# Performance work log

Measured on AMD Instinct MI355X. Metric: run time of the kernel, lower is better.

The kernel has to match this reference:

```python
import jax, jax.numpy as jnp
import numpy as np

D_MODEL = 1024
D_FF = 4096
EPS = 1e-5


def layer_norm(x, gamma, beta):
    mu = jnp.mean(x, axis=-1, keepdims=True)
    var = jnp.var(x, axis=-1, keepdims=True)
    return (x - mu) * jax.lax.rsqrt(var + EPS) * gamma + beta


def attention(x_q, x_kv, WQ, WK, WV, causal):
    Q = x_q @ WQ          # [B,Sq,D]
    K = x_kv @ WK         # [B,Sk,D]
    V = x_kv @ WV
    scale = 1.0 / jnp.sqrt(jnp.asarray(Q.shape[-1], Q.dtype))
    scores = jnp.einsum('bqd,bkd->bqk', Q, K) * scale
    if causal:
        Sq, Sk = scores.shape[-2], scores.shape[-1]
        mask = jnp.triu(jnp.full((Sq, Sk), -jnp.inf, scores.dtype), k=1)
        scores = scores + mask
    attn = jax.nn.softmax(scores, axis=-1)
    return jnp.einsum('bqk,bkd->bqd', attn, V)


def setup_inputs() -> dict:
    key = jax.random.key(0)
    ks = jax.random.split(key, 16)
    B, S = 4, 2048
    s = 0.02
    inp = {
        'y': jax.random.normal(ks[0], (B, S, D_MODEL), jnp.float32),
        'Z': jax.random.normal(ks[1], (B, S, D_MODEL), jnp.float32),
        'WQ1': jax.random.normal(ks[2], (D_MODEL, D_MODEL), jnp.float32) * s,
        'WK1': jax.random.normal(ks[3], (D_MODEL, D_MODEL), jnp.float32) * s,
        'WV1': jax.random.normal(ks[4], (D_MODEL, D_MODEL), jnp.float32) * s,
        'WQ2': jax.random.normal(ks[5], (D_MODEL, D_MODEL), jnp.float32) * s,
        'WK2': jax.random.normal(ks[6], (D_MODEL, D_MODEL), jnp.float32) * s,
        'WV2': jax.random.normal(ks[7], (D_MODEL, D_MODEL), jnp.float32) * s,
        'W_ff1': jax.random.normal(ks[8], (D_MODEL, D_FF), jnp.float32) * s,
        'b_ff1': jnp.zeros((D_FF,), jnp.float32),
        'W_ff2': jax.random.normal(ks[9], (D_FF, D_MODEL), jnp.float32) * s,
        'b_ff2': jnp.zeros((D_MODEL,), jnp.float32),
        'g1': jnp.ones((D_MODEL,), jnp.float32), 'be1': jnp.zeros((D_MODEL,), jnp.float32),
        'g2': jnp.ones((D_MODEL,), jnp.float32), 'be2': jnp.zeros((D_MODEL,), jnp.float32),
        'g3': jnp.ones((D_MODEL,), jnp.float32), 'be3': jnp.zeros((D_MODEL,), jnp.float32),
    }
    return inp


def reference(y, Z, WQ1, WK1, WV1, WQ2, WK2, WV2, W_ff1, b_ff1, W_ff2, b_ff2,
              g1, be1, g2, be2, g3, be3):
    # masked self-attention + add&norm
    y = layer_norm(y + attention(y, y, WQ1, WK1, WV1, causal=True), g1, be1)
    # cross-attention + add&norm
    y = layer_norm(y + attention(y, Z, WQ2, WK2, WV2, causal=False), g2, be2)
    # FFN + add&norm
    h = jax.nn.relu(y @ W_ff1 + b_ff1) @ W_ff2 + b_ff2
    y = layer_norm(y + h, g3, be3)
    return y
```

## Files before the change

### kernel.cpp

```cpp
#include <hip/hip_runtime.h>
#include <cstddef>

typedef unsigned short u16;
typedef __attribute__((ext_vector_type(8))) short bf16x8;
typedef __attribute__((ext_vector_type(4))) float f32x4;

__device__ __forceinline__ u16 f2bf(float f) {
  union { float f; unsigned u; } x; x.f = f;
  unsigned r = x.u + 0x7fffu + ((x.u >> 16) & 1u);
  return (u16)(r >> 16);
}
__device__ __forceinline__ float bf2f(u16 h) {
  union { unsigned u; float f; } x; x.u = ((unsigned)h) << 16;
  return x.f;
}

__device__ __forceinline__ void gll16(const u16* g, u16* ldsbase) {
  __builtin_amdgcn_global_load_lds(
      (const __attribute__((address_space(1))) void*)g,
      (__attribute__((address_space(3))) void*)ldsbase, 16, 0, 0);
}

__global__ __launch_bounds__(256) void f32_to_bf16(const float* __restrict__ in,
                                                   u16* __restrict__ out, size_t n) {
  size_t i = (size_t)blockIdx.x * 256 + threadIdx.x;
  if (i < n) out[i] = f2bf(in[i]);
}

__global__ __launch_bounds__(256) void transpose_f32_bf16(const float* __restrict__ in,
                                                          u16* __restrict__ out,
                                                          int R, int C) {
  __shared__ float tile[32][33];
  int c0 = blockIdx.x * 32, r0 = blockIdx.y * 32;
  int tx = threadIdx.x & 31, ty = threadIdx.x >> 5;
  #pragma unroll
  for (int i = ty; i < 32; i += 8)
    tile[i][tx] = in[(size_t)(r0 + i) * C + c0 + tx];
  __syncthreads();
  #pragma unroll
  for (int i = ty; i < 32; i += 8)
    out[(size_t)(c0 + i) * R + r0 + tx] = f2bf(tile[tx][i]);
}

enum { EPI_F32 = 0, EPI_BF16 = 1, EPI_BF16_SCALE = 2,
       EPI_BIAS_RELU_BF16 = 3, EPI_BIAS_F32 = 4 };
enum { MODE_FULL = 0, MODE_TRI = 1, MODE_CAUSAL_K = 2 };

template <int EPI, int MODE>
__global__ __launch_bounds__(512) void gemm256(
    const u16* __restrict__ A, const u16* __restrict__ Bt,
    void* __restrict__ C0, const float* __restrict__ bias,
    int K, int lda, int ldb, int ldc,
    long long sA, long long sB, long long sC)
{
  __shared__ __align__(16) u16 lA[2][256 * 64];
  __shared__ __align__(16) u16 lB[2][256 * 64];

  const unsigned gx = gridDim.x, gxy = gridDim.x * gridDim.y;
  unsigned id = blockIdx.x + gx * blockIdx.y + gxy * blockIdx.z;
  const unsigned nb = gxy * gridDim.z;
  unsigned p = id;
  if ((nb & 7u) == 0u) p = (id & 7u) * (nb >> 3) + (id >> 3);
  int z, mi, ni;
  if constexpr (MODE == MODE_TRI) {
    z = (int)(p / gxy);
    int r = (int)(p % gxy);
    int m = 0;
    while ((m + 1) * (m + 2) / 2 <= r) m++;
    mi = m; ni = r - m * (m + 1) / 2;
  } else {
    z = (int)(p / gxy);
    const unsigned rem = p % gxy;
    mi = (int)(rem / gx);
    ni = (int)(rem % gx);
  }
  const int m0 = mi * 256, n0 = ni * 256;

  A  += (long long)z * sA;
  Bt += (long long)z * sB;

  int NT = K >> 6;
  if constexpr (MODE == MODE_CAUSAL_K) NT = (m0 + 256) >> 6;

  const int t    = threadIdx.x;
  const int lane = t & 63;
  const int wave = t >> 6;
  const int wr   = wave >> 2;
  const int wc   = wave & 3;
  const int quad = lane >> 4;
  const int lrow = lane & 15;

  const int srow = lane >> 3;
  const int scol = ((lane & 7) ^ srow) * 8;
  const u16* gAp = A  + (size_t)(m0 + wave * 8 + srow) * lda + scol;
  const u16* gBp = Bt + (size_t)(n0 + wave * 8 + srow) * ldb + scol;
  const size_t a64 = (size_t)64 * lda, b64 = (size_t)64 * ldb;
  const int lw = wave * 512;

  const int pg0 = (quad ^ (lrow & 7)) * 8;
  const int pg1 = pg0 ^ 32;
  const int rA = (wr * 128 + lrow) * 64;
  const int rB = (wc * 64 + lrow) * 64;

  f32x4 acc[8][4];
  const f32x4 zero = {0.f, 0.f, 0.f, 0.f};
  #pragma unroll
  for (int i = 0; i < 8; i++)
    #pragma unroll
    for (int j = 0; j < 4; j++) acc[i][j] = zero;

  auto stage = [&](int b, int s, int kt) {
    const int k = kt * 64;
    if (s == 0) {
      gll16(gBp + k,            &lB[b][lw]);
      gll16(gBp + k + b64,      &lB[b][4096 + lw]);
    } else if (s == 1) {
      gll16(gBp + k + 2 * b64,  &lB[b][8192 + lw]);
      gll16(gBp + k + 3 * b64,  &lB[b][12288 + lw]);
    } else if (s == 2) {
      gll16(gAp + k,            &lA[b][lw]);
      gll16(gAp + k + a64,      &lA[b][4096 + lw]);
    } else {
      gll16(gAp + k + 2 * a64,  &lA[b][8192 + lw]);
      gll16(gAp + k + 3 * a64,  &lA[b][12288 + lw]);
    }
  };

  stage(0, 0, 0); stage(0, 1, 0); stage(0, 2, 0); stage(0, 3, 0);
  if (NT > 1) {
    stage(1, 0, 1); stage(1, 1, 1); stage(1, 2, 1);
    asm volatile("s_waitcnt vmcnt(6)" ::: "memory");
  } else {
    asm volatile("s_waitcnt vmcnt(0)" ::: "memory");
  }
  __builtin_amdgcn_s_barrier();

  bf16x8 af[4][2], bfr[4][2];

  for (int kt = 0; kt < NT; ++kt) {
    const int bsel = kt & 1;
    const u16* sa = &lA[bsel][0];
    const u16* sb = &lB[bsel][0];

    #pragma unroll
    for (int mf = 0; mf < 4; ++mf) {
      af[mf][0] = *(const bf16x8*)(sa + rA + mf * 1024 + pg0);
      af[mf][1] = *(const bf16x8*)(sa + rA + mf * 1024 + pg1);
    }
    if (wc < 2) {
      #pragma unroll
      for (int nf = 0; nf < 4; ++nf) {
        bfr[nf][0] = *(const bf16x8*)(sb + rB + nf * 1024 + pg0);
        bfr[nf][1] = *(const bf16x8*)(sb + rB + nf * 1024 + pg1);
      }
    } else {
      #pragma unroll
      for (int nf = 0; nf < 2; ++nf) {
        bfr[nf][0] = *(const bf16x8*)(sb + rB + nf * 1024 + pg0);
        bfr[nf][1] = *(const bf16x8*)(sb + rB + nf * 1024 + pg1);
      }
    }
    if (kt + 1 < NT) stage(bsel ^ 1, 3, kt + 1);
    __builtin_amdgcn_s_barrier();
    asm volatile("s_waitcnt lgkmcnt(0)" ::: "memory");
    __builtin_amdgcn_sched_barrier(0);
    __builtin_amdgcn_s_setprio(1);
    #pragma unroll
    for (int mf = 0; mf < 4; ++mf)
      #pragma unroll
      for (int nf = 0; nf < 2; ++nf) {
        acc[mf][nf] = __builtin_amdgcn_mfma_f32_16x16x32_bf16(bfr[nf][0], af[mf][0], acc[mf][nf], 0, 0, 0);
        acc[mf][nf] = __builtin_amdgcn_mfma_f32_16x16x32_bf16(bfr[nf][1], af[mf][1], acc[mf][nf], 0, 0, 0);
      }
    __builtin_amdgcn_s_setprio(0);
    __builtin_amdgcn_s_barrier();

    if (wc >= 2) {
      #pragma unroll
      for (int nf = 2; nf < 4; ++nf) {
        bfr[nf][0] = *(const bf16x8*)(sb + rB + nf * 1024 + pg0);
        bfr[nf][1] = *(const bf16x8*)(sb + rB + nf * 1024 + pg1);
      }
    }
    if (kt + 2 < NT) stage(bsel, 0, kt + 2);
    __builtin_amdgcn_s_barrier();
    asm volatile("s_waitcnt lgkmcnt(0)" ::: "memory");
    __builtin_amdgcn_sched_barrier(0);
    __builtin_amdgcn_s_setprio(1);
    #pragma unroll
    for (int mf = 0; mf < 4; ++mf)
      #pragma unroll
      for (int nf = 2; nf < 4; ++nf) {
        acc[mf][nf] = __builtin_amdgcn_mfma_f32_16x16x32_bf16(bfr[nf][0], af[mf][0], acc[mf][nf], 0, 0, 0);
        acc[mf][nf] = __builtin_amdgcn_mfma_f32_16x16x32_bf16(bfr[nf][1], af[mf][1], acc[mf][nf], 0, 0, 0);
      }
    __builtin_amdgcn_s_setprio(0);
    __builtin_amdgcn_s_barrier();

    #pragma unroll
    for (int mf = 0; mf < 4; ++mf) {
      af[mf][0] = *(const bf16x8*)(sa + rA + (mf + 4) * 1024 + pg0);
      af[mf][1] = *(const bf16x8*)(sa + rA + (mf + 4) * 1024 + pg1);
    }
    if (kt + 2 < NT) stage(bsel, 1, kt + 2);
    __builtin_amdgcn_s_barrier();
    asm volatile("s_waitcnt lgkmcnt(0)" ::: "memory");
    __builtin_amdgcn_sched_barrier(0);
    __builtin_amdgcn_s_setprio(1);
    #pragma unroll
    for (int mf = 0; mf < 4; ++mf)
      #pragma unroll
      for (int nf = 2; nf < 4; ++nf) {
        acc[mf + 4][nf] = __builtin_amdgcn_mfma_f32_16x16x32_bf16(bfr[nf][0], af[mf][0], acc[mf + 4][nf], 0, 0, 0);
        acc[mf + 4][nf] = __builtin_amdgcn_mfma_f32_16x16x32_bf16(bfr[nf][1], af[mf][1], acc[mf + 4][nf], 0, 0, 0);
      }
    __builtin_amdgcn_s_setprio(0);
    __builtin_amdgcn_s_barrier();

    if (kt + 2 < NT) {
      stage(bsel, 2, kt + 2);
      asm volatile("s_waitcnt vmcnt(6)" ::: "memory");
    } else if (kt + 1 < NT) {
      asm volatile("s_waitcnt vmcnt(0)" ::: "memory");
    }
    __builtin_amdgcn_s_barrier();
    __builtin_amdgcn_s_setprio(1);
    #pragma unroll
    for (int mf = 0; mf < 4; ++mf)
      #pragma unroll
      for (int nf = 0; nf < 2; ++nf) {
        acc[mf + 4][nf] = __builtin_amdgcn_mfma_f32_16x16x32_bf16(bfr[nf][0], af[mf][0], acc[mf + 4][nf], 0, 0, 0);
        acc[mf + 4][nf] = __builtin_amdgcn_mfma_f32_16x16x32_bf16(bfr[nf][1], af[mf][1], acc[mf + 4][nf], 0, 0, 0);
      }
    __builtin_amdgcn_s_setprio(0);
    __builtin_amdgcn_s_barrier();
  }

  const size_t zoff = (size_t)((long long)z * sC);
  #pragma unroll
  for (int mf = 0; mf < 8; ++mf) {
    #pragma unroll
    for (int nf = 0; nf < 4; ++nf) {
      const size_t m  = (size_t)(m0 + wr * 128 + mf * 16 + lrow);
      const size_t nc = (size_t)(n0 + wc * 64 + nf * 16 + quad * 4);
      const size_t idx = zoff + m * (size_t)ldc + nc;
      f32x4 v = acc[mf][nf];
      if constexpr (EPI == EPI_F32) {
        *(float4*)((float*)C0 + idx) = make_float4(v[0], v[1], v[2], v[3]);
      } else if constexpr (EPI == EPI_BF16) {
        ushort4 o; o.x = f2bf(v[0]); o.y = f2bf(v[1]); o.z = f2bf(v[2]); o.w = f2bf(v[3]);
        *(ushort4*)((u16*)C0 + idx) = o;
      } else if constexpr (EPI == EPI_BF16_SCALE) {
        ushort4 o;
        o.x = f2bf(v[0] * 0.03125f); o.y = f2bf(v[1] * 0.03125f);
        o.z = f2bf(v[2] * 0.03125f); o.w = f2bf(v[3] * 0.03125f);
        *(ushort4*)((u16*)C0 + idx) = o;
      } else if constexpr (EPI == EPI_BIAS_RELU_BF16) {
        const float4 bb = *(const float4*)(bias + nc);
        float y0 = v[0] + bb.x, y1 = v[1] + bb.y, y2 = v[2] + bb.z, y3 = v[3] + bb.w;
        ushort4 o;
        o.x = f2bf(y0 > 0.f ? y0 : 0.f); o.y = f2bf(y1 > 0.f ? y1 : 0.f);
        o.z = f2bf(y2 > 0.f ? y2 : 0.f); o.w = f2bf(y3 > 0.f ? y3 : 0.f);
        *(ushort4*)((u16*)C0 + idx) = o;
      } else {
        const float4 bb = *(const float4*)(bias + nc);
        *(float4*)((float*)C0 + idx) =
            make_float4(v[0] + bb.x, v[1] + bb.y, v[2] + bb.z, v[3] + bb.w);
      }
    }
  }
}

__global__ __launch_bounds__(256) void softmax_bf16(u16* __restrict__ SP, int causal) {
  __shared__ float red[8];
  const int row = blockIdx.x;
  const int q = row & 2047;
  u16* p = SP + (size_t)row * 2048;
  const int t = threadIdx.x;
  const int base = t * 8;
  const int limit = causal ? (q + 1) : 2048;

  uint4 raw = *(const uint4*)(p + base);
  unsigned w[4] = {raw.x, raw.y, raw.z, raw.w};
  float v[8];
  #pragma unroll
  for (int j = 0; j < 4; j++) {
    union { unsigned u; float f; } lo, hi;
    lo.u = w[j] << 16; hi.u = w[j] & 0xffff0000u;
    v[2 * j] = lo.f; v[2 * j + 1] = hi.f;
  }
  #pragma unroll
  for (int j = 0; j < 8; j++) if (base + j >= limit) v[j] = -3.4e38f;

  float mx = v[0];
  #pragma unroll
  for (int j = 1; j < 8; j++) mx = fmaxf(mx, v[j]);
  #pragma unroll
  for (int o = 32; o > 0; o >>= 1) mx = fmaxf(mx, __shfl_down(mx, o));
  if ((t & 63) == 0) red[t >> 6] = mx;
  __syncthreads();
  mx = fmaxf(fmaxf(red[0], red[1]), fmaxf(red[2], red[3]));

  float s = 0.f;
  #pragma unroll
  for (int j = 0; j < 8; j++) { float e = __expf(v[j] - mx); v[j] = e; s += e; }
  #pragma unroll
  for (int o = 32; o > 0; o >>= 1) s += __shfl_down(s, o);
  if ((t & 63) == 0) red[4 + (t >> 6)] = s;
  __syncthreads();
  const float inv = 1.f / (red[4] + red[5] + red[6] + red[7]);

  unsigned o4[4];
  #pragma unroll
  for (int j = 0; j < 4; j++)
    o4[j] = (unsigned)f2bf(v[2 * j] * inv) | ((unsigned)f2bf(v[2 * j + 1] * inv) << 16);
  *(uint4*)(p + base) = make_uint4(o4[0], o4[1], o4[2], o4[3]);
}

template <int ABF>
__global__ __launch_bounds__(256) void ln_residual(const void* __restrict__ a_,
                                                   const float* __restrict__ b,
                                                   const float* __restrict__ g,
                                                   const float* __restrict__ be,
                                                   float* __restrict__ outf,
                                                   u16* __restrict__ outb) {
  __shared__ float red[8];
  const size_t base = (size_t)blockIdx.x * 1024;
  const int t = threadIdx.x;
  const int i0 = t * 4;

  float va[4];
  if constexpr (ABF) {
    const ushort4 h = *(const ushort4*)((const u16*)a_ + base + i0);
    va[0] = bf2f(h.x); va[1] = bf2f(h.y); va[2] = bf2f(h.z); va[3] = bf2f(h.w);
  } else {
    const float4 f = *(const float4*)((const float*)a_ + base + i0);
    va[0] = f.x; va[1] = f.y; va[2] = f.z; va[3] = f.w;
  }
  const float4 vb = *(const float4*)(b + base + i0);
  float v[4] = {va[0] + vb.x, va[1] + vb.y, va[2] + vb.z, va[3] + vb.w};

  float s = v[0] + v[1] + v[2] + v[3];
  #pragma unroll
  for (int o = 32; o > 0; o >>= 1) s += __shfl_down(s, o);
  if ((t & 63) == 0) red[t >> 6] = s;
  __syncthreads();
  const float mean = (red[0] + red[1] + red[2] + red[3]) * (1.f / 1024.f);

  float qq = 0.f;
  #pragma unroll
  for (int i = 0; i < 4; i++) { float d = v[i] - mean; qq += d * d; }
  #pragma unroll
  for (int o = 32; o > 0; o >>= 1) qq += __shfl_down(qq, o);
  if ((t & 63) == 0) red[4 + (t >> 6)] = qq;
  __syncthreads();
  const float rstd = rsqrtf((red[4] + red[5] + red[6] + red[7]) * (1.f / 1024.f) + 1e-5f);

  const float4 gg = *(const float4*)(g + i0);
  const float4 bb = *(const float4*)(be + i0);
  float y0 = (v[0] - mean) * rstd * gg.x + bb.x;
  float y1 = (v[1] - mean) * rstd * gg.y + bb.y;
  float y2 = (v[2] - mean) * rstd * gg.z + bb.z;
  float y3 = (v[3] - mean) * rstd * gg.w + bb.w;
  if (outf) *(float4*)(outf + base + i0) = make_float4(y0, y1, y2, y3);
  if (outb) {
    ushort4 o4; o4.x = f2bf(y0); o4.y = f2bf(y1); o4.z = f2bf(y2); o4.w = f2bf(y3);
    *(ushort4*)(outb + base + i0) = o4;
  }
}

extern "C" void kernel_launch(void* const* d_in, const int* in_sizes, int n_in,
                              void* d_out, int out_size, void* d_ws, size_t ws_size,
                              hipStream_t stream)
{
  const float* y_in = (const float*)d_in[0];
  const float* Z_in = (const float*)d_in[1];
  const float* WQ1  = (const float*)d_in[2];
  const float* WK1  = (const float*)d_in[3];
  const float* WV1  = (const float*)d_in[4];
  const float* WQ2  = (const float*)d_in[5];
  const float* WK2  = (const float*)d_in[6];
  const float* WV2  = (const float*)d_in[7];
  const float* Wff1 = (const float*)d_in[8];
  const float* bff1 = (const float*)d_in[9];
  const float* Wff2 = (const float*)d_in[10];
  const float* bff2 = (const float*)d_in[11];
  const float* g1  = (const float*)d_in[12];
  const float* be1 = (const float*)d_in[13];
  const float* g2  = (const float*)d_in[14];
  const float* be2 = (const float*)d_in[15];
  const float* g3  = (const float*)d_in[16];
  const float* be3 = (const float*)d_in[17];
  (void)in_sizes; (void)n_in; (void)out_size;

  constexpr int Bn = 4, S = 2048, D = 1024, DF = 4096;
  constexpr long long BS = (long long)Bn * S;
  const long long SD = (long long)S * D;
  const long long SS = (long long)S * S;
  const long long SD2 = (long long)S * 2 * D;

  char* ws = (char*)d_ws;
  size_t off = 0;
  auto alloc = [&](size_t bytes) -> char* {
    char* p = ws + off;
    off += (bytes + 255) & ~(size_t)255;
    return p;
  };

  u16* wq1t  = (u16*)alloc((size_t)D * D * 2);
  u16* wk1t  = (u16*)alloc((size_t)D * D * 2);
  u16* wv1t  = (u16*)alloc((size_t)D * D * 2);
  u16* wq2t  = (u16*)alloc((size_t)D * D * 2);
  u16* wk2t  = (u16*)alloc((size_t)D * D * 2);
  u16* wv2t  = (u16*)alloc((size_t)D * D * 2);
  u16* wff1t = (u16*)alloc((size_t)D * DF * 2);
  u16* wff2t = (u16*)alloc((size_t)D * DF * 2);
  u16* ybf   = (u16*)alloc((size_t)BS * D * 2);
  u16* zbf   = (u16*)alloc((size_t)BS * D * 2);
  u16* QKb   = (u16*)alloc((size_t)BS * 2 * D * 2);
  u16* Vtb   = (u16*)alloc((size_t)D * BS * 2);
  u16* SPb   = (u16*)alloc((size_t)Bn * S * S * 2);
  float* attnF = (float*)alloc((size_t)BS * D * 4);
  u16*   y1b = ybf;
  u16*   y2b = zbf;
  u16*   Hb  = QKb;
  float* Fb  = attnF;

  if (off > ws_size) return;

  const dim3 blk(256);
  const dim3 blk512(512);

  f32_to_bf16<<<dim3((unsigned)((BS * D) / 256)), blk, 0, stream>>>(y_in, ybf, (size_t)BS * D);
  f32_to_bf16<<<dim3((unsigned)((BS * D) / 256)), blk, 0, stream>>>(Z_in, zbf, (size_t)BS * D);
  transpose_f32_bf16<<<dim3(D / 32, D / 32), blk, 0, stream>>>(WQ1, wq1t, D, D);
  transpose_f32_bf16<<<dim3(D / 32, D / 32), blk, 0, stream>>>(WK1, wk1t, D, D);
  transpose_f32_bf16<<<dim3(D / 32, D / 32), blk, 0, stream>>>(WV1, wv1t, D, D);
  transpose_f32_bf16<<<dim3(D / 32, D / 32), blk, 0, stream>>>(WQ2, wq2t, D, D);
  transpose_f32_bf16<<<dim3(D / 32, D / 32), blk, 0, stream>>>(WK2, wk2t, D, D);
  transpose_f32_bf16<<<dim3(D / 32, D / 32), blk, 0, stream>>>(WV2, wv2t, D, D);
  transpose_f32_bf16<<<dim3(DF / 32, D / 32), blk, 0, stream>>>(Wff1, wff1t, D, DF);
  transpose_f32_bf16<<<dim3(D / 32, DF / 32), blk, 0, stream>>>(Wff2, wff2t, DF, D);

  gemm256<EPI_BF16, MODE_FULL><<<dim3(2 * D / 256, BS / 256, 1), blk512, 0, stream>>>(
      ybf, wq1t, QKb, nullptr, D, D, D, 2 * D, 0, 0, 0);
  gemm256<EPI_BF16, MODE_FULL><<<dim3((unsigned)(BS / 256), D / 256, 1), blk512, 0, stream>>>(
      wv1t, ybf, Vtb, nullptr, D, D, D, (int)BS, 0, 0, 0);
  gemm256<EPI_BF16_SCALE, MODE_TRI><<<dim3(36, 1, Bn), blk512, 0, stream>>>(
      QKb, QKb + D, SPb, nullptr, D, 2 * D, 2 * D, S, SD2, SD2, SS);
  softmax_bf16<<<dim3((unsigned)(Bn * S)), blk, 0, stream>>>(SPb, 1);
  gemm256<EPI_F32, MODE_CAUSAL_K><<<dim3(D / 256, S / 256, Bn), blk512, 0, stream>>>(
      SPb, Vtb, attnF, nullptr, S, S, (int)BS, D, SS, S, SD);
  ln_residual<0><<<dim3((unsigned)BS), blk, 0, stream>>>(y_in, attnF, g1, be1, nullptr, y1b);

  gemm256<EPI_BF16, MODE_FULL><<<dim3(D / 256, BS / 256, 1), blk512, 0, stream>>>(
      y1b, wq2t, QKb, nullptr, D, D, D, 2 * D, 0, 0, 0);
  gemm256<EPI_BF16, MODE_FULL><<<dim3(D / 256, BS / 256, 1), blk512, 0, stream>>>(
      zbf, wk2t, QKb + D, nullptr, D, D, D, 2 * D, 0, 0, 0);
  gemm256<EPI_BF16, MODE_FULL><<<dim3((unsigned)(BS / 256), D / 256, 1), blk512, 0, stream>>>(
      wv2t, zbf, Vtb, nullptr, D, D, D, (int)BS, 0, 0, 0);
  gemm256<EPI_BF16_SCALE, MODE_FULL><<<dim3(S / 256, S / 256, Bn), blk512, 0, stream>>>(
      QKb, QKb + D, SPb, nullptr, D, 2 * D, 2 * D, S, SD2, SD2, SS);
  softmax_bf16<<<dim3((unsigned)(Bn * S)), blk, 0, stream>>>(SPb, 0);
  gemm256<EPI_F32, MODE_FULL><<<dim3(D / 256, S / 256, Bn), blk512, 0, stream>>>(
      SPb, Vtb, attnF, nullptr, S, S, (int)BS, D, SS, S, SD);
  ln_residual<1><<<dim3((unsigned)BS), blk, 0, stream>>>(y1b, attnF, g2, be2, nullptr, y2b);

  gemm256<EPI_BIAS_RELU_BF16, MODE_FULL><<<dim3(DF / 256, BS / 256, 1), blk512, 0, stream>>>(
      y2b, wff1t, Hb, bff1, D, D, D, DF, 0, 0, 0);
  gemm256<EPI_BIAS_F32, MODE_FULL><<<dim3(D / 256, BS / 256, 1), blk512, 0, stream>>>(
      Hb, wff2t, Fb, bff2, DF, DF, DF, D, 0, 0, 0);
  ln_residual<1><<<dim3((unsigned)BS), blk, 0, stream>>>(y2b, Fb, g3, be3, (float*)d_out, nullptr);
}
```

Before: 870.7 us.

## Templatize GEMM tile shape, add triple-buffered pipeline, merge Q/K GEMMs, trim softmax

Makes the GEMM tile shape a template parameter (BM×BN) and adds a triple-buffered pipeline for the non-256×256 tiles. The 256×256 loop is simplified to two phases per k-step. Smaller tiles go to the skinny GEMMs (V projection, PV, FFN2, causal QK) to fill more CUs, and the cross-attention Q and K projections are merged into one launch via a dsplit operand switch. Causal softmax now skips loads beyond the diagonal and stores only up to the 256-aligned block boundary. The risks are lower per-block data reuse with the smaller tiles and pipeline synchronisation bugs in the rewritten schedule.

```diff
diff --git a/kernel.cpp b/kernel.cpp
--- a/kernel.cpp
+++ b/kernel.cpp
@@ -46,15 +46,24 @@
        EPI_BIAS_RELU_BF16 = 3, EPI_BIAS_F32 = 4 };
 enum { MODE_FULL = 0, MODE_TRI = 1, MODE_CAUSAL_K = 2 };
 
-template <int EPI, int MODE>
+template <int EPI, int MODE, int BM, int BN>
 __global__ __launch_bounds__(512) void gemm256(
     const u16* __restrict__ A, const u16* __restrict__ Bt,
     void* __restrict__ C0, const float* __restrict__ bias,
+    const u16* __restrict__ A2, const u16* __restrict__ B2, int dsplit,
     int K, int lda, int ldb, int ldc,
     long long sA, long long sB, long long sC)
 {
-  __shared__ __align__(16) u16 lA[2][256 * 64];
-  __shared__ __align__(16) u16 lB[2][256 * 64];
+  constexpr int WM  = BM / 128;
+  constexpr int WN  = 8 / WM;
+  constexpr int CPW = BN / WN;
+  constexpr int NF  = CPW / 16;
+  constexpr int nBr = BN / 64;
+  constexpr int nAr = BM / 64;
+  constexpr int NBUF = (BM == 256 && BN == 256) ? 2 : 3;
+
+  __shared__ __align__(16) u16 lA[NBUF][BM * 64];
+  __shared__ __align__(16) u16 lB[NBUF][BN * 64];
 
   const unsigned gx = gridDim.x, gxy = gridDim.x * gridDim.y;
   unsigned id = blockIdx.x + gx * blockIdx.y + gxy * blockIdx.z;
@@ -66,27 +75,37 @@
     z = (int)(p / gxy);
     int r = (int)(p % gxy);
     int m = 0;
-    while ((m + 1) * (m + 2) / 2 <= r) m++;
-    mi = m; ni = r - m * (m + 1) / 2;
+    if constexpr (BN == 256) {
+      while ((m + 1) * (m + 2) / 2 <= r) m++;
+      mi = m; ni = r - m * (m + 1) / 2;
+    } else {
+      while ((m + 1) * (m + 2) <= r) m++;
+      mi = m; ni = r - m * (m + 1);
+    }
   } else {
     z = (int)(p / gxy);
     const unsigned rem = p % gxy;
     mi = (int)(rem / gx);
     ni = (int)(rem % gx);
   }
-  const int m0 = mi * 256, n0 = ni * 256;
+  if (dsplit && ni >= dsplit) {
+    A = A2; Bt = B2;
+    C0 = (void*)((u16*)C0 + (size_t)dsplit * BN);
+    ni -= dsplit;
+  }
+  const int m0 = mi * BM, n0 = ni * BN;
 
   A  += (long long)z * sA;
   Bt += (long long)z * sB;
 
   int NT = K >> 6;
-  if constexpr (MODE == MODE_CAUSAL_K) NT = (m0 + 256) >> 6;
+  if constexpr (MODE == MODE_CAUSAL_K) NT = (m0 + BM) >> 6;
 
   const int t    = threadIdx.x;
   const int lane = t & 63;
   const int wave = t >> 6;
-  const int wr   = wave >> 2;
-  const int wc   = wave & 3;
+  const int wr   = (WM == 1) ? 0 : (wave >> 2);
+  const int wc   = (WM == 1) ? wave : (wave & 3);
   const int quad = lane >> 4;
   const int lrow = lane & 15;
 
@@ -100,149 +119,162 @@
   const int pg0 = (quad ^ (lrow & 7)) * 8;
   const int pg1 = pg0 ^ 32;
   const int rA = (wr * 128 + lrow) * 64;
-  const int rB = (wc * 64 + lrow) * 64;
-
-  f32x4 acc[8][4];
+  const int rB = (wc * CPW + lrow) * 64;
+
+  f32x4 acc[8][NF];
   const f32x4 zero = {0.f, 0.f, 0.f, 0.f};
   #pragma unroll
   for (int i = 0; i < 8; i++)
     #pragma unroll
-    for (int j = 0; j < 4; j++) acc[i][j] = zero;
-
-  auto stage = [&](int b, int s, int kt) {
-    const int k = kt * 64;
-    if (s == 0) {
-      gll16(gBp + k,            &lB[b][lw]);
-      gll16(gBp + k + b64,      &lB[b][4096 + lw]);
-    } else if (s == 1) {
-      gll16(gBp + k + 2 * b64,  &lB[b][8192 + lw]);
-      gll16(gBp + k + 3 * b64,  &lB[b][12288 + lw]);
-    } else if (s == 2) {
-      gll16(gAp + k,            &lA[b][lw]);
-      gll16(gAp + k + a64,      &lA[b][4096 + lw]);
+    for (int j = 0; j < NF; j++) acc[i][j] = zero;
+
+  bf16x8 X[4][2];
+  bf16x8 Y[4][2];
+  bf16x8 bfr[NF][2];
+
+  auto rdX = [&](const u16* s) {
+    #pragma unroll
+    for (int mf = 0; mf < 4; ++mf) {
+      X[mf][0] = *(const bf16x8*)(s + rA + mf * 1024 + pg0);
+      X[mf][1] = *(const bf16x8*)(s + rA + mf * 1024 + pg1);
+    }
+  };
+  auto rdY = [&](const u16* s) {
+    #pragma unroll
+    for (int mf = 0; mf < 4; ++mf) {
+      Y[mf][0] = *(const bf16x8*)(s + rA + (mf + 4) * 1024 + pg0);
+      Y[mf][1] = *(const bf16x8*)(s + rA + (mf + 4) * 1024 + pg1);
+    }
+  };
+  auto rdB = [&](const u16* s) {
+    #pragma unroll
+    for (int nf = 0; nf < NF; ++nf) {
+      bfr[nf][0] = *(const bf16x8*)(s + rB + nf * 1024 + pg0);
+      bfr[nf][1] = *(const bf16x8*)(s + rB + nf * 1024 + pg1);
+    }
+  };
+
+  if constexpr (NBUF == 2) {
+    auto stageB2 = [&](int b, int kt) {
+      const int k = kt * 64;
+      gll16(gBp + k,           &lB[b][lw]);
+      gll16(gBp + k + b64,     &lB[b][4096 + lw]);
+      gll16(gBp + k + 2 * b64, &lB[b][8192 + lw]);
+      gll16(gBp + k + 3 * b64, &lB[b][12288 + lw]);
+    };
+    auto stageA2 = [&](int b, int kt) {
+      const int k = kt * 64;
+      gll16(gAp + k,           &lA[b][lw]);
+      gll16(gAp + k + a64,     &lA[b][4096 + lw]);
+      gll16(gAp + k + 2 * a64, &lA[b][8192 + lw]);
+      gll16(gAp + k + 3 * a64, &lA[b][12288 + lw]);
+    };
+
+    stageB2(0, 0); stageA2(0, 0);
+    if (NT > 1) {
+      stageB2(1, 1);
+      asm volatile("s_waitcnt vmcnt(4)" ::: "memory");
     } else {
-      gll16(gAp + k + 2 * a64,  &lA[b][8192 + lw]);
-      gll16(gAp + k + 3 * a64,  &lA[b][12288 + lw]);
-    }
-  };
-
-  stage(0, 0, 0); stage(0, 1, 0); stage(0, 2, 0); stage(0, 3, 0);
-  if (NT > 1) {
-    stage(1, 0, 1); stage(1, 1, 1); stage(1, 2, 1);
-    asm volatile("s_waitcnt vmcnt(6)" ::: "memory");
+      asm volatile("s_waitcnt vmcnt(0)" ::: "memory");
+    }
+    __builtin_amdgcn_s_barrier();
+
+    for (int kt = 0; kt < NT; ++kt) {
+      const int bsel = kt & 1;
+      const u16* sa = &lA[bsel][0];
+      const u16* sb = &lB[bsel][0];
+
+      rdX(sa); rdB(sb);
+      if (kt + 1 < NT) stageA2(bsel ^ 1, kt + 1);
+      asm volatile("s_waitcnt lgkmcnt(0)" ::: "memory");
+      __builtin_amdgcn_sched_barrier(0);
+      __builtin_amdgcn_s_setprio(1);
+      #pragma unroll
+      for (int mf = 0; mf < 4; ++mf)
+        #pragma unroll
+        for (int nf = 0; nf < 4; ++nf) {
+          acc[mf][nf] = __builtin_amdgcn_mfma_f32_16x16x32_bf16(bfr[nf][0], X[mf][0], acc[mf][nf], 0, 0, 0);
+          acc[mf][nf] = __builtin_amdgcn_mfma_f32_16x16x32_bf16(bfr[nf][1], X[mf][1], acc[mf][nf], 0, 0, 0);
+        }
+      __builtin_amdgcn_s_setprio(0);
+      __builtin_amdgcn_s_barrier();
+
+      rdY(sa);
+      if (kt + 2 < NT) stageB2(bsel, kt + 2);
+      asm volatile("s_waitcnt lgkmcnt(0)" ::: "memory");
+      __builtin_amdgcn_sched_barrier(0);
+      __builtin_amdgcn_s_setprio(1);
+      #pragma unroll
+      for (int mf = 0; mf < 4; ++mf)
+        #pragma unroll
+        for (int nf = 0; nf < 4; ++nf) {
+          acc[mf + 4][nf] = __builtin_amdgcn_mfma_f32_16x16x32_bf16(bfr[nf][0], Y[mf][0], acc[mf + 4][nf], 0, 0, 0);
+          acc[mf + 4][nf] = __builtin_amdgcn_mfma_f32_16x16x32_bf16(bfr[nf][1], Y[mf][1], acc[mf + 4][nf], 0, 0, 0);
+        }
+      __builtin_amdgcn_s_setprio(0);
+      if (kt + 2 < NT)      asm volatile("s_waitcnt vmcnt(4)" ::: "memory");
+      else if (kt + 1 < NT) asm volatile("s_waitcnt vmcnt(0)" ::: "memory");
+      __builtin_amdgcn_s_barrier();
+    }
   } else {
-    asm volatile("s_waitcnt vmcnt(0)" ::: "memory");
-  }
-  __builtin_amdgcn_s_barrier();
-
-  bf16x8 af[4][2], bfr[4][2];
-
-  for (int kt = 0; kt < NT; ++kt) {
-    const int bsel = kt & 1;
-    const u16* sa = &lA[bsel][0];
-    const u16* sb = &lB[bsel][0];
-
-    #pragma unroll
-    for (int mf = 0; mf < 4; ++mf) {
-      af[mf][0] = *(const bf16x8*)(sa + rA + mf * 1024 + pg0);
-      af[mf][1] = *(const bf16x8*)(sa + rA + mf * 1024 + pg1);
-    }
-    if (wc < 2) {
+    u16 *a0 = &lA[0][0], *a1 = &lA[1][0], *a2 = &lA[2][0];
+    u16 *b0 = &lB[0][0], *b1 = &lB[1][0], *b2 = &lB[2][0];
+    auto stage6 = [&](u16* ba, u16* bb, int kt) {
+      const int k = kt * 64;
       #pragma unroll
-      for (int nf = 0; nf < 4; ++nf) {
-        bfr[nf][0] = *(const bf16x8*)(sb + rB + nf * 1024 + pg0);
-        bfr[nf][1] = *(const bf16x8*)(sb + rB + nf * 1024 + pg1);
-      }
+      for (int s = 0; s < nBr; ++s)
+        gll16(gBp + k + (size_t)s * b64, bb + s * 4096 + lw);
+      #pragma unroll
+      for (int s = 0; s < nAr; ++s)
+        gll16(gAp + k + (size_t)s * a64, ba + s * 4096 + lw);
+    };
+
+    stage6(a0, b0, 0);
+    if (NT > 1) {
+      stage6(a1, b1, 1);
+      asm volatile("s_waitcnt vmcnt(6)" ::: "memory");
     } else {
+      asm volatile("s_waitcnt vmcnt(0)" ::: "memory");
+    }
+    __builtin_amdgcn_s_barrier();
+
+    for (int kt = 0; kt < NT; ++kt) {
+      rdX(a0); rdY(a0); rdB(b0);
+      if (kt + 2 < NT) stage6(a2, b2, kt + 2);
+      asm volatile("s_waitcnt lgkmcnt(0)" ::: "memory");
+      __builtin_amdgcn_sched_barrier(0);
+      __builtin_amdgcn_s_setprio(1);
       #pragma unroll
-      for (int nf = 0; nf < 2; ++nf) {
-        bfr[nf][0] = *(const bf16x8*)(sb + rB + nf * 1024 + pg0);
-        bfr[nf][1] = *(const bf16x8*)(sb + rB + nf * 1024 + pg1);
-      }
-    }
-    if (kt + 1 < NT) stage(bsel ^ 1, 3, kt + 1);
-    __builtin_amdgcn_s_barrier();
-    asm volatile("s_waitcnt lgkmcnt(0)" ::: "memory");
-    __builtin_amdgcn_sched_barrier(0);
-    __builtin_amdgcn_s_setprio(1);
-    #pragma unroll
-    for (int mf = 0; mf < 4; ++mf)
+      for (int mf = 0; mf < 4; ++mf)
+        #pragma unroll
+        for (int nf = 0; nf < 2; ++nf) {
+          acc[mf][nf] = __builtin_amdgcn_mfma_f32_16x16x32_bf16(bfr[nf][0], X[mf][0], acc[mf][nf], 0, 0, 0);
+          acc[mf][nf] = __builtin_amdgcn_mfma_f32_16x16x32_bf16(bfr[nf][1], X[mf][1], acc[mf][nf], 0, 0, 0);
+        }
       #pragma unroll
-      for (int nf = 0; nf < 2; ++nf) {
-        acc[mf][nf] = __builtin_amdgcn_mfma_f32_16x16x32_bf16(bfr[nf][0], af[mf][0], acc[mf][nf], 0, 0, 0);
-        acc[mf][nf] = __builtin_amdgcn_mfma_f32_16x16x32_bf16(bfr[nf][1], af[mf][1], acc[mf][nf], 0, 0, 0);
-      }
-    __builtin_amdgcn_s_setprio(0);
-    __builtin_amdgcn_s_barrier();
-
-    if (wc >= 2) {
-      #pragma unroll
-      for (int nf = 2; nf < 4; ++nf) {
-        bfr[nf][0] = *(const bf16x8*)(sb + rB + nf * 1024 + pg0);
-        bfr[nf][1] = *(const bf16x8*)(sb + rB + nf * 1024 + pg1);
-      }
-    }
-    if (kt + 2 < NT) stage(bsel, 0, kt + 2);
-    __builtin_amdgcn_s_barrier();
-    asm volatile("s_waitcnt lgkmcnt(0)" ::: "memory");
-    __builtin_amdgcn_sched_barrier(0);
-    __builtin_amdgcn_s_setprio(1);
-    #pragma unroll
-    for (int mf = 0; mf < 4; ++mf)
-      #pragma unroll
-      for (int nf = 2; nf < 4; ++nf) {
-        acc[mf][nf] = __builtin_amdgcn_mfma_f32_16x16x32_bf16(bfr[nf][0], af[mf][0], acc[mf][nf], 0, 0, 0);
-        acc[mf][nf] = __builtin_amdgcn_mfma_f32_16x16x32_bf16(bfr[nf][1], af[mf][1], acc[mf][nf], 0, 0, 0);
-      }
-    __builtin_amdgcn_s_setprio(0);
-    __builtin_amdgcn_s_barrier();
-
-    #pragma unroll
-    for (int mf = 0; mf < 4; ++mf) {
-      af[mf][0] = *(const bf16x8*)(sa + rA + (mf + 4) * 1024 + pg0);
-      af[mf][1] = *(const bf16x8*)(sa + rA + (mf + 4) * 1024 + pg1);
-    }
-    if (kt + 2 < NT) stage(bsel, 1, kt + 2);
-    __builtin_amdgcn_s_barrier();
-    asm volatile("s_waitcnt lgkmcnt(0)" ::: "memory");
-    __builtin_amdgcn_sched_barrier(0);
-    __builtin_amdgcn_s_setprio(1);
-    #pragma unroll
-    for (int mf = 0; mf < 4; ++mf)
-      #pragma unroll
-      for (int nf = 2; nf < 4; ++nf) {
-        acc[mf + 4][nf] = __builtin_amdgcn_mfma_f32_16x16x32_bf16(bfr[nf][0], af[mf][0], acc[mf + 4][nf], 0, 0, 0);
-        acc[mf + 4][nf] = __builtin_amdgcn_mfma_f32_16x16x32_bf16(bfr[nf][1], af[mf][1], acc[mf + 4][nf], 0, 0, 0);
-      }
-    __builtin_amdgcn_s_setprio(0);
-    __builtin_amdgcn_s_barrier();
-
-    if (kt + 2 < NT) {
-      stage(bsel, 2, kt + 2);
-      asm volatile("s_waitcnt vmcnt(6)" ::: "memory");
-    } else if (kt + 1 < NT) {
-      asm volatile("s_waitcnt vmcnt(0)" ::: "memory");
-    }
-    __builtin_amdgcn_s_barrier();
-    __builtin_amdgcn_s_setprio(1);
-    #pragma unroll
-    for (int mf = 0; mf < 4; ++mf)
-      #pragma unroll
-      for (int nf = 0; nf < 2; ++nf) {
-        acc[mf + 4][nf] = __builtin_amdgcn_mfma_f32_16x16x32_bf16(bfr[nf][0], af[mf][0], acc[mf + 4][nf], 0, 0, 0);
-        acc[mf + 4][nf] = __builtin_amdgcn_mfma_f32_16x16x32_bf16(bfr[nf][1], af[mf][1], acc[mf + 4][nf], 0, 0, 0);
-      }
-    __builtin_amdgcn_s_setprio(0);
-    __builtin_amdgcn_s_barrier();
+      for (int mf = 0; mf < 4; ++mf)
+        #pragma unroll
+        for (int nf = 0; nf < 2; ++nf) {
+          acc[mf + 4][nf] = __builtin_amdgcn_mfma_f32_16x16x32_bf16(bfr[nf][0], Y[mf][0], acc[mf + 4][nf], 0, 0, 0);
+          acc[mf + 4][nf] = __builtin_amdgcn_mfma_f32_16x16x32_bf16(bfr[nf][1], Y[mf][1], acc[mf + 4][nf], 0, 0, 0);
+        }
+      __builtin_amdgcn_s_setprio(0);
+      if (kt + 2 < NT)      asm volatile("s_waitcnt vmcnt(6)" ::: "memory");
+      else if (kt + 1 < NT) asm volatile("s_waitcnt vmcnt(0)" ::: "memory");
+      __builtin_amdgcn_s_barrier();
+      u16* tp;
+      tp = a0; a0 = a1; a1 = a2; a2 = tp;
+      tp = b0; b0 = b1; b1 = b2; b2 = tp;
+    }
   }
 
   const size_t zoff = (size_t)((long long)z * sC);
   #pragma unroll
   for (int mf = 0; mf < 8; ++mf) {
     #pragma unroll
-    for (int nf = 0; nf < 4; ++nf) {
+    for (int nf = 0; nf < NF; ++nf) {
       const size_t m  = (size_t)(m0 + wr * 128 + mf * 16 + lrow);
-      const size_t nc = (size_t)(n0 + wc * 64 + nf * 16 + quad * 4);
+      const size_t nc = (size_t)(n0 + wc * CPW + nf * 16 + quad * 4);
       const size_t idx = zoff + m * (size_t)ldc + nc;
       f32x4 v = acc[mf][nf];
       if constexpr (EPI == EPI_F32) {
@@ -278,19 +310,25 @@
   u16* p = SP + (size_t)row * 2048;
   const int t = threadIdx.x;
   const int base = t * 8;
-  const int limit = causal ? (q + 1) : 2048;
-
-  uint4 raw = *(const uint4*)(p + base);
-  unsigned w[4] = {raw.x, raw.y, raw.z, raw.w};
+  const int limit  = causal ? (q + 1) : 2048;
+  const int wlimit = causal ? (((q >> 8) + 1) << 8) : 2048;
+
   float v[8];
-  #pragma unroll
-  for (int j = 0; j < 4; j++) {
-    union { unsigned u; float f; } lo, hi;
-    lo.u = w[j] << 16; hi.u = w[j] & 0xffff0000u;
-    v[2 * j] = lo.f; v[2 * j + 1] = hi.f;
-  }
-  #pragma unroll
-  for (int j = 0; j < 8; j++) if (base + j >= limit) v[j] = -3.4e38f;
+  if (base < limit) {
+    uint4 raw = *(const uint4*)(p + base);
+    unsigned w[4] = {raw.x, raw.y, raw.z, raw.w};
+    #pragma unroll
+    for (int j = 0; j < 4; j++) {
+      union { unsigned u; float f; } lo, hi;
+      lo.u = w[j] << 16; hi.u = w[j] & 0xffff0000u;
+      v[2 * j] = lo.f; v[2 * j + 1] = hi.f;
+    }
+    #pragma unroll
+    for (int j = 0; j < 8; j++) if (base + j >= limit) v[j] = -3.4e38f;
+  } else {
+    #pragma unroll
+    for (int j = 0; j < 8; j++) v[j] = -3.4e38f;
+  }
 
   float mx = v[0];
   #pragma unroll
@@ -310,11 +348,13 @@
   __syncthreads();
   const float inv = 1.f / (red[4] + red[5] + red[6] + red[7]);
 
-  unsigned o4[4];
-  #pragma unroll
-  for (int j = 0; j < 4; j++)
-    o4[j] = (unsigned)f2bf(v[2 * j] * inv) | ((unsigned)f2bf(v[2 * j + 1] * inv) << 16);
-  *(uint4*)(p + base) = make_uint4(o4[0], o4[1], o4[2], o4[3]);
+  if (base < wlimit) {
+    unsigned o4[4];
+    #pragma unroll
+    for (int j = 0; j < 4; j++)
+      o4[j] = (unsigned)f2bf(v[2 * j] * inv) | ((unsigned)f2bf(v[2 * j + 1] * inv) << 16);
+    *(uint4*)(p + base) = make_uint4(o4[0], o4[1], o4[2], o4[3]);
+  }
 }
 
 template <int ABF>
@@ -442,33 +482,31 @@
   transpose_f32_bf16<<<dim3(DF / 32, D / 32), blk, 0, stream>>>(Wff1, wff1t, D, DF);
   transpose_f32_bf16<<<dim3(D / 32, DF / 32), blk, 0, stream>>>(Wff2, wff2t, DF, D);
 
-  gemm256<EPI_BF16, MODE_FULL><<<dim3(2 * D / 256, BS / 256, 1), blk512, 0, stream>>>(
-      ybf, wq1t, QKb, nullptr, D, D, D, 2 * D, 0, 0, 0);
-  gemm256<EPI_BF16, MODE_FULL><<<dim3((unsigned)(BS / 256), D / 256, 1), blk512, 0, stream>>>(
-      wv1t, ybf, Vtb, nullptr, D, D, D, (int)BS, 0, 0, 0);
-  gemm256<EPI_BF16_SCALE, MODE_TRI><<<dim3(36, 1, Bn), blk512, 0, stream>>>(
-      QKb, QKb + D, SPb, nullptr, D, 2 * D, 2 * D, S, SD2, SD2, SS);
+  gemm256<EPI_BF16, MODE_FULL, 256, 256><<<dim3(2 * D / 256, BS / 256, 1), blk512, 0, stream>>>(
+      ybf, wq1t, QKb, nullptr, nullptr, nullptr, 0, D, D, D, 2 * D, 0, 0, 0);
+  gemm256<EPI_BF16, MODE_FULL, 128, 256><<<dim3((unsigned)(BS / 256), D / 128, 1), blk512, 0, stream>>>(
+      wv1t, ybf, Vtb, nullptr, nullptr, nullptr, 0, D, D, D, (int)BS, 0, 0, 0);
+  gemm256<EPI_BF16_SCALE, MODE_TRI, 256, 128><<<dim3(72, 1, Bn), blk512, 0, stream>>>(
+      QKb, QKb + D, SPb, nullptr, nullptr, nullptr, 0, D, 2 * D, 2 * D, S, SD2, SD2, SS);
   softmax_bf16<<<dim3((unsigned)(Bn * S)), blk, 0, stream>>>(SPb, 1);
-  gemm256<EPI_F32, MODE_CAUSAL_K><<<dim3(D / 256, S / 256, Bn), blk512, 0, stream>>>(
-      SPb, Vtb, attnF, nullptr, S, S, (int)BS, D, SS, S, SD);
+  gemm256<EPI_F32, MODE_CAUSAL_K, 256, 128><<<dim3(D / 128, S / 256, Bn), blk512, 0, stream>>>(
+      SPb, Vtb, attnF, nullptr, nullptr, nullptr, 0, S, S, (int)BS, D, SS, S, SD);
   ln_residual<0><<<dim3((unsigned)BS), blk, 0, stream>>>(y_in, attnF, g1, be1, nullptr, y1b);
 
-  gemm256<EPI_BF16, MODE_FULL><<<dim3(D / 256, BS / 256, 1), blk512, 0, stream>>>(
-      y1b, wq2t, QKb, nullptr, D, D, D, 2 * D, 0, 0, 0);
-  gemm256<EPI_BF16, MODE_FULL><<<dim3(D / 256, BS / 256, 1), blk512, 0, stream>>>(
-      zbf, wk2t, QKb + D, nullptr, D, D, D, 2 * D, 0, 0, 0);
-  gemm256<EPI_BF16, MODE_FULL><<<dim3((unsigned)(BS / 256), D / 256, 1), blk512, 0, stream>>>(
-      wv2t, zbf, Vtb, nullptr, D, D, D, (int)BS, 0, 0, 0);
-  gemm256<EPI_BF16_SCALE, MODE_FULL><<<dim3(S / 256, S / 256, Bn), blk512, 0, stream>>>(
-      QKb, QKb + D, SPb, nullptr, D, 2 * D, 2 * D, S, SD2, SD2, SS);
+  gemm256<EPI_BF16, MODE_FULL, 256, 128><<<dim3(2 * D / 128, BS / 256, 1), blk512, 0, stream>>>(
+      y1b, wq2t, QKb, nullptr, zbf, wk2t, 8, D, D, D, 2 * D, 0, 0, 0);
+  gemm256<EPI_BF16, MODE_FULL, 128, 256><<<dim3((unsigned)(BS / 256), D / 128, 1), blk512, 0, stream>>>(
+      wv2t, zbf, Vtb, nullptr, nullptr, nullptr, 0, D, D, D, (int)BS, 0, 0, 0);
+  gemm256<EPI_BF16_SCALE, MODE_FULL, 256, 256><<<dim3(S / 256, S / 256, Bn), blk512, 0, stream>>>(
+      QKb, QKb + D, SPb, nullptr, nullptr, nullptr, 0, D, 2 * D, 2 * D, S, SD2, SD2, SS);
   softmax_bf16<<<dim3((unsigned)(Bn * S)), blk, 0, stream>>>(SPb, 0);
-  gemm256<EPI_F32, MODE_FULL><<<dim3(D / 256, S / 256, Bn), blk512, 0, stream>>>(
-      SPb, Vtb, attnF, nullptr, S, S, (int)BS, D, SS, S, SD);
+  gemm256<EPI_F32, MODE_FULL, 256, 128><<<dim3(D / 128, S / 256, Bn), blk512, 0, stream>>>(
+      SPb, Vtb, attnF, nullptr, nullptr, nullptr, 0, S, S, (int)BS, D, SS, S, SD);
   ln_residual<1><<<dim3((unsigned)BS), blk, 0, stream>>>(y1b, attnF, g2, be2, nullptr, y2b);
 
-  gemm256<EPI_BIAS_RELU_BF16, MODE_FULL><<<dim3(DF / 256, BS / 256, 1), blk512, 0, stream>>>(
-      y2b, wff1t, Hb, bff1, D, D, D, DF, 0, 0, 0);
-  gemm256<EPI_BIAS_F32, MODE_FULL><<<dim3(D / 256, BS / 256, 1), blk512, 0, stream>>>(
-      Hb, wff2t, Fb, bff2, DF, DF, DF, D, 0, 0, 0);
+  gemm256<EPI_BIAS_RELU_BF16, MODE_FULL, 256, 256><<<dim3(DF / 256, BS / 256, 1), blk512, 0, stream>>>(
+      y2b, wff1t, Hb, bff1, nullptr, nullptr, 0, D, D, D, DF, 0, 0, 0);
+  gemm256<EPI_BIAS_F32, MODE_FULL, 256, 128><<<dim3(D / 128, BS / 256, 1), blk512, 0, stream>>>(
+      Hb, wff2t, Fb, bff2, nullptr, nullptr, 0, DF, DF, DF, D, 0, 0, 0);
   ln_residual<1><<<dim3((unsigned)BS), blk, 0, stream>>>(y2b, Fb, g3, be3, (float*)d_out, nullptr);
 }
```

Result: faster. 712.9 us (-18.1%).
